# Optimization experiments

Measured on AMD Instinct MI355X. Metric: run time of the kernel, lower is better.

Reference implementation:

```python
import jax, jax.numpy as jnp
import numpy as np

B, T, P = 32, 40, 12
E, H = 2048, 1024
A_DIM, ACT_DIM = 9, 8


def _xavier(key, shape):
    fan_out, fan_in = shape
    lim = float(np.sqrt(6.0 / (fan_in + fan_out)))
    return jax.random.uniform(key, shape, jnp.float32, -lim, lim)


def setup_inputs() -> dict:
    key = jax.random.key(0)
    ks = jax.random.split(key, 8)
    return {
        "feature": jax.random.normal(ks[0], (B, T, P, E), jnp.float32),
        "W_embed": _xavier(ks[1], (H, E)),
        "b_embed": jnp.zeros((H,), jnp.float32),
        "W_ih": _xavier(ks[2], (3 * H, H)),
        "W_hh": _xavier(ks[3], (3 * H, H)),
        "b_ih": jnp.zeros((3 * H,), jnp.float32),
        "b_hh": jnp.zeros((3 * H,), jnp.float32),
        "W_act": _xavier(ks[4], (A_DIM, H)),
        "b_act": jnp.zeros((A_DIM,), jnp.float32),
        "W_activ": _xavier(ks[5], (ACT_DIM, H)),
        "b_activ": jnp.zeros((ACT_DIM,), jnp.float32),
    }


def reference(feature, W_embed, b_embed, W_ih, W_hh, b_ih, b_hh,
              W_act, b_act, W_activ, b_activ):
    # embed: Linear + Tanh -> [B, T, P, H]
    x = jnp.tanh(jnp.einsum('btpe,he->btph', feature, W_embed) + b_embed)
    # precompute input-side GRU gates for all timesteps: [B, T, P, 3H]
    gx = jnp.einsum('btph,gh->btpg', x, W_ih) + b_ih

    def step(h, gx_t):  # h: [B, P, H], gx_t: [B, P, 3H]
        gh = jnp.einsum('bph,gh->bpg', h, W_hh) + b_hh
        xr, xz, xn = jnp.split(gx_t, 3, axis=-1)
        hr, hz, hn = jnp.split(gh, 3, axis=-1)
        r = jax.nn.sigmoid(xr + hr)
        z = jax.nn.sigmoid(xz + hz)
        n = jnp.tanh(xn + r * hn)
        h_new = (1.0 - z) * n + z * h
        return h_new, h_new

    h0 = jnp.zeros((feature.shape[0], feature.shape[2], W_hh.shape[1]), feature.dtype)
    _, hs = jax.lax.scan(step, h0, jnp.moveaxis(gx, 1, 0))  # hs: [T, B, P, H]
    hiddens = jnp.moveaxis(hs, 0, 1)  # [B, T, P, H]

    # per-person action logits; torch loop order is (batch, time, person)
    action_logits = (jnp.einsum('btph,ah->btpa', hiddens, W_act) + b_act
                     ).reshape(-1, W_act.shape[0])
    # MaxPool2d((P,1)) over person axis, then Linear
    pooled = hiddens.max(axis=2)  # [B, T, H]
    activity_logits = (jnp.einsum('bth,ah->bta', pooled, W_activ) + b_activ
                       ).reshape(-1, W_activ.shape[0])
    return action_logits, activity_logits
```

## Files before the change

### kernel.cpp

```cpp
#include <hip/hip_runtime.h>
#include <cstdint>

#define B_ 32
#define T_ 40
#define P_ 12
#define E_ 2048
#define H_ 1024
#define BP 384
#define M_ 15360

typedef _Float16 f16;
typedef _Float16 f16x8 __attribute__((ext_vector_type(8)));
typedef float f32x4 __attribute__((ext_vector_type(4)));

__device__ __forceinline__ void cp16(const void* g, void* l) {
    auto gp = (const __attribute__((address_space(1))) uint32_t*)(uintptr_t)g;
    auto lp = (__attribute__((address_space(3))) uint32_t*)(uint32_t)(uintptr_t)l;
    __builtin_amdgcn_global_load_lds(gp, lp, 16, 0, 0);
}

__device__ __forceinline__ float fast_tanh(float x) {
    return 1.f - 2.f / (__expf(2.f * x) + 1.f);
}
__device__ __forceinline__ float fast_sig(float x) {
    return 1.f / (1.f + __expf(-x));
}

__global__ __launch_bounds__(256) void cvt_f32_f16(const float* __restrict__ in,
                                                   f16* __restrict__ out, int n8) {
    int i = blockIdx.x * 256 + threadIdx.x;
    if (i >= n8) return;
    const float4* in4 = (const float4*)in;
    float4 a = in4[2 * i], b = in4[2 * i + 1];
    f16x8 o = {(f16)a.x, (f16)a.y, (f16)a.z, (f16)a.w,
               (f16)b.x, (f16)b.y, (f16)b.z, (f16)b.w};
    ((f16x8*)out)[i] = o;
}

template <int EPI>
__global__ __launch_bounds__(256) void gemm128(const f16* __restrict__ A,
                                               const f16* __restrict__ Bm,
                                               const float* __restrict__ bias,
                                               f16* __restrict__ out, int K, int N) {
    __shared__ f16 As[128 * 32];
    __shared__ f16 Bs[128 * 32];
    const int tid = threadIdx.x;
    const int w = tid >> 6, l = tid & 63;
    const int wm = w >> 1, wn = w & 1;
    const long arow0 = (long)blockIdx.x * 128;
    const long brow0 = (long)blockIdx.y * 128;
    const int srow = l >> 2, scol = (l & 3) * 8;

    f32x4 acc[4][4] = {};

    for (int k0 = 0; k0 < K; k0 += 32) {
        __syncthreads();
#pragma unroll
        for (int s = 0; s < 2; ++s) {
            int slice = w + s * 4;
            cp16(A + (arow0 + slice * 16 + srow) * (long)K + k0 + scol,
                 (void*)(As + slice * 512));
            cp16(Bm + (brow0 + slice * 16 + srow) * (long)K + k0 + scol,
                 (void*)(Bs + slice * 512));
        }
        __syncthreads();
        f16x8 af[4], bf[4];
#pragma unroll
        for (int i = 0; i < 4; ++i)
            af[i] = *(const f16x8*)(As + (wm * 64 + i * 16 + (l & 15)) * 32 + (l >> 4) * 8);
#pragma unroll
        for (int j = 0; j < 4; ++j)
            bf[j] = *(const f16x8*)(Bs + (wn * 64 + j * 16 + (l & 15)) * 32 + (l >> 4) * 8);
#pragma unroll
        for (int i = 0; i < 4; ++i)
#pragma unroll
            for (int j = 0; j < 4; ++j)
                acc[i][j] = __builtin_amdgcn_mfma_f32_16x16x32_f16(af[i], bf[j], acc[i][j], 0, 0, 0);
    }

    const int colq = l & 15, rowq = (l >> 4) * 4;
#pragma unroll
    for (int i = 0; i < 4; ++i)
#pragma unroll
        for (int j = 0; j < 4; ++j)
#pragma unroll
            for (int r = 0; r < 4; ++r) {
                long m = arow0 + wm * 64 + i * 16 + rowq + r;
                int n = (int)brow0 + wn * 64 + j * 16 + colq;
                float v = acc[i][j][r] + bias[n];
                if (EPI == 0) {
                    out[m * N + n] = (f16)fast_tanh(v);
                } else {
                    int b = (int)(m / (T_ * P_));
                    int rem = (int)(m % (T_ * P_));
                    int t = rem / P_, p = rem % P_;
                    out[((long)t * BP + b * P_ + p) * N + n] = (f16)v;
                }
            }
}

__global__ __launch_bounds__(256) void gru_step(const f16* __restrict__ h16_in,
                                                f16* __restrict__ h16_out,
                                                float* __restrict__ h32,
                                                const f16* __restrict__ Whh,
                                                const float* __restrict__ b_hh,
                                                const f16* __restrict__ gx16,
                                                f16* __restrict__ hid16, int t) {
    __shared__ f16 As[32 * 32];
    __shared__ f16 Bs[3 * 64 * 32];
    const int tid = threadIdx.x;
    const int w = tid >> 6, l = tid & 63;
    const int m0 = blockIdx.x * 32, n0 = blockIdx.y * 64;
    const int srow = l >> 2, scol = (l & 3) * 8;

    f32x4 acc[3][2] = {};

    for (int k0 = 0; k0 < H_; k0 += 32) {
        __syncthreads();
        if (w < 2)
            cp16(h16_in + (m0 + w * 16 + srow) * H_ + k0 + scol, (void*)(As + w * 512));
#pragma unroll
        for (int q3 = 0; q3 < 3; ++q3) {
            int s = w + q3 * 4;
            int g = s >> 2, q = s & 3;
            cp16(Whh + (long)(g * H_ + n0 + q * 16 + srow) * H_ + k0 + scol,
                 (void*)(Bs + (g * 64 + q * 16) * 32));
        }
        __syncthreads();
        f16x8 af[2], bf[3];
#pragma unroll
        for (int i = 0; i < 2; ++i)
            af[i] = *(const f16x8*)(As + (i * 16 + (l & 15)) * 32 + (l >> 4) * 8);
#pragma unroll
        for (int g = 0; g < 3; ++g)
            bf[g] = *(const f16x8*)(Bs + (g * 64 + w * 16 + (l & 15)) * 32 + (l >> 4) * 8);
#pragma unroll
        for (int g = 0; g < 3; ++g)
#pragma unroll
            for (int i = 0; i < 2; ++i)
                acc[g][i] = __builtin_amdgcn_mfma_f32_16x16x32_f16(af[i], bf[g], acc[g][i], 0, 0, 0);
    }

    const int col = n0 + w * 16 + (l & 15);
    const long gxbase = (long)t * BP * 3072;
    const float bhr = b_hh[col], bhz = b_hh[H_ + col], bhn = b_hh[2 * H_ + col];
#pragma unroll
    for (int i = 0; i < 2; ++i)
#pragma unroll
        for (int r = 0; r < 4; ++r) {
            int m = m0 + i * 16 + (l >> 4) * 4 + r;
            float hr = acc[0][i][r] + bhr;
            float hz = acc[1][i][r] + bhz;
            float hn = acc[2][i][r] + bhn;
            long gxrow = gxbase + (long)m * 3072;
            float xr = (float)gx16[gxrow + col];
            float xz = (float)gx16[gxrow + H_ + col];
            float xn = (float)gx16[gxrow + 2 * H_ + col];
            float rr = fast_sig(xr + hr);
            float zz = fast_sig(xz + hz);
            float nn = fast_tanh(xn + rr * hn);
            float hp = h32[m * H_ + col];
            float hnew = (1.f - zz) * nn + zz * hp;
            h32[m * H_ + col] = hnew;
            h16_out[m * H_ + col] = (f16)hnew;
            int b = m / P_, p = m % P_;
            hid16[(((long)b * T_ + t) * P_ + p) * H_ + col] = (f16)hnew;
        }
}

#define GRU_GRID 256
#define GRU_THREADS 384
#define GRU_BLDS (48 * 1024 * 2)
#define GRU_ALDS (4 * 96 * 64 * 2)
#define GRU_LDS (GRU_BLDS + GRU_ALDS)
#define FLAG_STRIDE 16

__global__ __launch_bounds__(GRU_THREADS) void gru_persistent(
        const f16* __restrict__ Whh, const float* __restrict__ bhh,
        const f16* __restrict__ gx16, f16* __restrict__ hid16,
        int* __restrict__ flags) {
    extern __shared__ char lds[];
    char* const Asb = lds + GRU_BLDS;

    const int tid = threadIdx.x;
    const int w = tid >> 6, l = tid & 63;
    const int q = l >> 4;

    const int bid = blockIdx.x;
    const int x = bid & 7;
    const int rg = x >> 1;
    const int nb = (x & 1) * 32 + (bid >> 3);
    const int m0 = rg * 96;
    const int j0 = nb * 16;

    for (int c = tid; c < 6144; c += GRU_THREADS) {
        int r = c >> 7;
        int kc = (c & 127) * 8;
        int grow = (r >> 4) * H_ + j0 + (r & 15);
        f16x8 v = *(const f16x8*)(Whh + (long)grow * H_ + kc);
        *(f16x8*)(lds + r * 2048 + ((kc * 2) ^ ((r & 7) << 4))) = v;
    }

    const int arow_l = w * 16 + (l & 15);
    int a_off[2], b_off[3][2];
#pragma unroll
    for (int sub = 0; sub < 2; ++sub) {
        a_off[sub] = arow_l * 128 + (((sub * 32 + q * 8) * 2) ^ ((arow_l & 7) << 4));
#pragma unroll
        for (int g = 0; g < 3; ++g) {
            int br = g * 16 + (l & 15);
            b_off[g][sub] = br * 2048 + (((sub * 32 + q * 8) * 2) ^ ((br & 7) << 4));
        }
    }
    const int swz = ((l & 7) ^ (l >> 3)) << 3;
    const int mA1 = m0 + w * 16 + (l >> 3);
    const int mA2 = mA1 + 8;
    const long srcA1 = ((long)(mA1 / P_) * T_ * P_ + (mA1 % P_)) * H_ + swz;
    const long srcA2 = ((long)(mA2 / P_) * T_ * P_ + (mA2 % P_)) * H_ + swz;

    const int col = j0 + (l & 15);
    const float bhr = bhh[col], bhz = bhh[H_ + col], bhn = bhh[2 * H_ + col];
    const int mrow = m0 + w * 16 + q * 4;
    long dstrow[4];
#pragma unroll
    for (int r = 0; r < 4; ++r) {
        int m = mrow + r;
        dstrow[r] = ((long)(m / P_) * T_ * P_ + (m % P_)) * H_ + col;
    }

    float hval[4] = {0.f, 0.f, 0.f, 0.f};

    f16 pgr[4], pgz[4], pgn[4];
#pragma unroll
    for (int r = 0; r < 4; ++r) {
        const long row = (long)(mrow + r) * 3072 + col;
        pgr[r] = gx16[row];
        pgz[r] = gx16[row + H_];
        pgn[r] = gx16[row + 2 * H_];
    }
    __syncthreads();

    for (int t = 0; t < T_; ++t) {
        f32x4 acc0 = {}, acc1 = {}, acc2 = {};

        if (t > 0) {
            if (w == 0) {
                const int* fp = flags + (((rg << 6) + l) * FLAG_STRIDE);
                while (__hip_atomic_load(fp, __ATOMIC_RELAXED,
                                         __HIP_MEMORY_SCOPE_AGENT) < t) {
                    __builtin_amdgcn_s_sleep(2);
                }
                __builtin_amdgcn_fence(__ATOMIC_ACQUIRE, "agent");
            }
            __syncthreads();

            const f16* __restrict__ hsrc = hid16 + (long)(t - 1) * (P_ * H_);

#pragma unroll
            for (int s = 0; s < 3; ++s) {
                char* b = Asb + s * 12288 + w * 2048;
                cp16(hsrc + srcA1 + s * 64, b);
                cp16(hsrc + srcA2 + s * 64, b + 1024);
            }

#pragma unroll
            for (int kk = 0; kk < 16; ++kk) {
                asm volatile("s_waitcnt lgkmcnt(0)" ::: "memory");
                if (kk < 13) {
                    const int s = kk + 3;
                    char* b = Asb + (s & 3) * 12288 + w * 2048;
                    cp16(hsrc + srcA1 + s * 64, b);
                    cp16(hsrc + srcA2 + s * 64, b + 1024);
                    asm volatile("s_waitcnt vmcnt(6)" ::: "memory");
                } else if (kk == 13) {
                    asm volatile("s_waitcnt vmcnt(4)" ::: "memory");
                } else if (kk == 14) {
                    asm volatile("s_waitcnt vmcnt(2)" ::: "memory");
                } else {
                    asm volatile("s_waitcnt vmcnt(0)" ::: "memory");
                }
                __builtin_amdgcn_sched_barrier(0);
                const char* Ab = Asb + (kk & 3) * 12288;
#pragma unroll
                for (int sub = 0; sub < 2; ++sub) {
                    f16x8 af  = *(const f16x8*)(Ab + a_off[sub]);
                    f16x8 bf0 = *(const f16x8*)(lds + b_off[0][sub] + kk * 128);
                    f16x8 bf1 = *(const f16x8*)(lds + b_off[1][sub] + kk * 128);
                    f16x8 bf2 = *(const f16x8*)(lds + b_off[2][sub] + kk * 128);
                    acc0 = __builtin_amdgcn_mfma_f32_16x16x32_f16(af, bf0, acc0, 0, 0, 0);
                    acc1 = __builtin_amdgcn_mfma_f32_16x16x32_f16(af, bf1, acc1, 0, 0, 0);
                    acc2 = __builtin_amdgcn_mfma_f32_16x16x32_f16(af, bf2, acc2, 0, 0, 0);
                }
            }
        }

        const long toff = (long)t * (P_ * H_);
#pragma unroll
        for (int r = 0; r < 4; ++r) {
            float hr = acc0[r] + bhr;
            float hz = acc1[r] + bhz;
            float hn = acc2[r] + bhn;
            float rr = fast_sig((float)pgr[r] + hr);
            float zz = fast_sig((float)pgz[r] + hz);
            float nn = fast_tanh((float)pgn[r] + rr * hn);
            float hnew = (1.f - zz) * nn + zz * hval[r];
            hval[r] = hnew;
            hid16[toff + dstrow[r]] = (f16)hnew;
        }

        if (t + 1 < T_) {
            const long gxb = (long)(t + 1) * BP * 3072 + col;
#pragma unroll
            for (int r = 0; r < 4; ++r) {
                const long row = gxb + (long)(mrow + r) * 3072;
                pgr[r] = gx16[row];
                pgz[r] = gx16[row + H_];
                pgn[r] = gx16[row + 2 * H_];
            }
        }

        __syncthreads();
        if (tid == 0) {
            __hip_atomic_store(flags + (((rg << 6) + nb) * FLAG_STRIDE), t + 1,
                               __ATOMIC_RELEASE, __HIP_MEMORY_SCOPE_AGENT);
        }
    }
}

__global__ __launch_bounds__(256) void logits_kernel(const f16* __restrict__ hid16,
                                                     const float* __restrict__ W_act,
                                                     const float* __restrict__ b_act,
                                                     const float* __restrict__ W_activ,
                                                     const float* __restrict__ b_activ,
                                                     float* __restrict__ out) {
    __shared__ f16 hs[P_ * H_];
    __shared__ float pooled[H_];
    const int bt = blockIdx.x;
    const int tid = threadIdx.x, w = tid >> 6, l = tid & 63;

    const f16x8* src = (const f16x8*)(hid16 + (long)bt * P_ * H_);
    f16x8* dst = (f16x8*)hs;
    for (int i = tid; i < P_ * H_ / 8; i += 256) dst[i] = src[i];
    __syncthreads();

    for (int i = tid; i < H_; i += 256) {
        float mx = (float)hs[i];
#pragma unroll
        for (int p = 1; p < P_; ++p) mx = fmaxf(mx, (float)hs[p * H_ + i]);
        pooled[i] = mx;
    }
    __syncthreads();

    for (int j = w; j < 108; j += 4) {
        int p = j / 9, a = j % 9;
        float s = 0.f;
#pragma unroll
        for (int it = 0; it < 16; ++it) {
            int idx = l + it * 64;
            s += (float)hs[p * H_ + idx] * W_act[a * H_ + idx];
        }
#pragma unroll
        for (int off = 32; off > 0; off >>= 1) s += __shfl_down(s, off);
        if (l == 0) out[((long)bt * P_ + p) * 9 + a] = s + b_act[a];
    }
    for (int j = w; j < 8; j += 4) {
        float s = 0.f;
#pragma unroll
        for (int it = 0; it < 16; ++it) {
            int idx = l + it * 64;
            s += pooled[idx] * W_activ[j * H_ + idx];
        }
#pragma unroll
        for (int off = 32; off > 0; off >>= 1) s += __shfl_down(s, off);
        if (l == 0) out[(long)M_ * 9 + (long)bt * 8 + j] = s + b_activ[j];
    }
}

extern "C" void kernel_launch(void* const* d_in, const int* in_sizes, int n_in,
                              void* d_out, int out_size, void* d_ws, size_t ws_size,
                              hipStream_t stream) {
    const float* feature = (const float*)d_in[0];
    const float* W_embed = (const float*)d_in[1];
    const float* b_embed = (const float*)d_in[2];
    const float* W_ih    = (const float*)d_in[3];
    const float* W_hh    = (const float*)d_in[4];
    const float* b_ih    = (const float*)d_in[5];
    const float* b_hh    = (const float*)d_in[6];
    const float* W_act   = (const float*)d_in[7];
    const float* b_act   = (const float*)d_in[8];
    const float* W_activ = (const float*)d_in[9];
    const float* b_activ = (const float*)d_in[10];
    float* out = (float*)d_out;

    char* ws = (char*)d_ws;
    size_t off = 0;
    auto alloc = [&](size_t bytes) {
        void* p = ws + off;
        off = (off + bytes + 255) & ~(size_t)255;
        return p;
    };
    f16*   feat16 = (f16*)alloc((size_t)M_ * E_ * 2);
    f16*   wE16   = (f16*)alloc((size_t)H_ * E_ * 2);
    f16*   wIH16  = (f16*)alloc((size_t)3 * H_ * H_ * 2);
    f16*   wHH16  = (f16*)alloc((size_t)3 * H_ * H_ * 2);
    f16*   x16    = (f16*)alloc((size_t)M_ * H_ * 2);
    f16*   gx16   = (f16*)alloc((size_t)M_ * 3 * H_ * 2);
    float* h32    = (float*)alloc((size_t)BP * H_ * 4);
    f16*   h16a   = (f16*)alloc((size_t)BP * H_ * 2);
    f16*   h16b   = (f16*)alloc((size_t)BP * H_ * 2);
    f16*   hid16  = (f16*)alloc((size_t)M_ * H_ * 2);
    int*   flags  = (int*)h32;
    (void)ws_size; (void)in_sizes; (void)n_in; (void)out_size;

    cvt_f32_f16<<<(M_ * E_) / 2048, 256, 0, stream>>>(feature, feat16, (M_ * E_) / 8);
    cvt_f32_f16<<<(H_ * E_) / 2048, 256, 0, stream>>>(W_embed, wE16, (H_ * E_) / 8);
    cvt_f32_f16<<<(3 * H_ * H_) / 2048, 256, 0, stream>>>(W_ih, wIH16, (3 * H_ * H_) / 8);
    cvt_f32_f16<<<(3 * H_ * H_) / 2048, 256, 0, stream>>>(W_hh, wHH16, (3 * H_ * H_) / 8);

    gemm128<0><<<dim3(M_ / 128, H_ / 128), 256, 0, stream>>>(feat16, wE16, b_embed, x16, E_, H_);
    gemm128<1><<<dim3(M_ / 128, (3 * H_) / 128), 256, 0, stream>>>(x16, wIH16, b_ih, gx16, H_, 3 * H_);

    hipMemsetAsync(h32, 0, (size_t)BP * H_ * 4 + (size_t)BP * H_ * 2, stream);

    (void)hipFuncSetAttribute(reinterpret_cast<const void*>(gru_persistent),
                              hipFuncAttributeMaxDynamicSharedMemorySize, GRU_LDS);
    const f16* p_whh = wHH16; const float* p_bhh = b_hh; const f16* p_gx = gx16;
    f16* p_hid = hid16; int* p_flags = flags;
    void* kargs[] = {&p_whh, &p_bhh, &p_gx, &p_hid, &p_flags};
    hipError_t cerr = hipLaunchCooperativeKernel(
        reinterpret_cast<const void*>(gru_persistent),
        dim3(GRU_GRID), dim3(GRU_THREADS), kargs, GRU_LDS, stream);
    if (cerr != hipSuccess) {
        for (int t = 0; t < T_; ++t) {
            const f16* hin = (t & 1) ? h16b : h16a;
            f16* hout = (t & 1) ? h16a : h16b;
            gru_step<<<dim3(BP / 32, H_ / 64), 256, 0, stream>>>(hin, hout, h32, wHH16, b_hh,
                                                                 gx16, hid16, t);
        }
    }

    logits_kernel<<<B_ * T_, 256, 0, stream>>>(hid16, W_act, b_act, W_activ, b_activ, out);
}
```

Before: 919.4 us.

## Double-buffer GEMM LDS loads, merge convert kernels, signal GRU flags earlier

The tiled GEMM now double-buffers its A and B tiles in LDS, prefetching the next K slice while MFMAs run on the current one. This cuts the barriers per iteration from two to one and aims to hide global-load latency. The four f32-to-f16 conversion launches are merged into one kernel to save launch overhead. In the persistent GRU, hidden-state stores become write-through and the step flag is released before the next gx prefetch, so dependent blocks can proceed sooner; the cost is double the GEMM LDS use and an explicit wait on store completion.

Result: no change. 929.5 us (+1.1%).

```diff
diff --git a/kernel.cpp b/kernel.cpp
--- a/kernel.cpp
+++ b/kernel.cpp
@@ -19,6 +19,11 @@
     __builtin_amdgcn_global_load_lds(gp, lp, 16, 0, 0);
 }
 
+__device__ __forceinline__ void store_wt(f16* p, f16 v) {
+    unsigned short u = __builtin_bit_cast(unsigned short, v);
+    asm volatile("global_store_short %0, %1, off sc0 sc1" :: "v"(p), "v"(u) : "memory");
+}
+
 __device__ __forceinline__ float fast_tanh(float x) {
     return 1.f - 2.f / (__expf(2.f * x) + 1.f);
 }
@@ -26,15 +31,28 @@
     return 1.f / (1.f + __expf(-x));
 }
 
-__global__ __launch_bounds__(256) void cvt_f32_f16(const float* __restrict__ in,
-                                                   f16* __restrict__ out, int n8) {
+#define CVT_N0 ((M_ * E_) / 8)
+#define CVT_N1 (CVT_N0 + (H_ * E_) / 8)
+#define CVT_N2 (CVT_N1 + (3 * H_ * H_) / 8)
+#define CVT_N3 (CVT_N2 + (3 * H_ * H_) / 8)
+__global__ __launch_bounds__(256) void cvt_all(const float* __restrict__ f,
+                                               const float* __restrict__ we,
+                                               const float* __restrict__ wih,
+                                               const float* __restrict__ whh,
+                                               f16* __restrict__ fo, f16* __restrict__ weo,
+                                               f16* __restrict__ wiho, f16* __restrict__ whho) {
     int i = blockIdx.x * 256 + threadIdx.x;
-    if (i >= n8) return;
-    const float4* in4 = (const float4*)in;
-    float4 a = in4[2 * i], b = in4[2 * i + 1];
+    if (i >= CVT_N3) return;
+    const float* src; f16* dst; int j;
+    if (i < CVT_N0)      { src = f;   dst = fo;   j = i; }
+    else if (i < CVT_N1) { src = we;  dst = weo;  j = i - CVT_N0; }
+    else if (i < CVT_N2) { src = wih; dst = wiho; j = i - CVT_N1; }
+    else                 { src = whh; dst = whho; j = i - CVT_N2; }
+    const float4* in4 = (const float4*)src;
+    float4 a = in4[2 * j], b = in4[2 * j + 1];
     f16x8 o = {(f16)a.x, (f16)a.y, (f16)a.z, (f16)a.w,
                (f16)b.x, (f16)b.y, (f16)b.z, (f16)b.w};
-    ((f16x8*)out)[i] = o;
+    ((f16x8*)dst)[j] = o;
 }
 
 template <int EPI>
@@ -42,8 +60,8 @@
                                                const f16* __restrict__ Bm,
                                                const float* __restrict__ bias,
                                                f16* __restrict__ out, int K, int N) {
-    __shared__ f16 As[128 * 32];
-    __shared__ f16 Bs[128 * 32];
+    __shared__ f16 As[2][128 * 32];
+    __shared__ f16 Bs[2][128 * 32];
     const int tid = threadIdx.x;
     const int w = tid >> 6, l = tid & 63;
     const int wm = w >> 1, wn = w & 1;
@@ -51,31 +69,46 @@
     const long brow0 = (long)blockIdx.y * 128;
     const int srow = l >> 2, scol = (l & 3) * 8;
 
+    const f16* aptr = A + (arow0 + srow) * (long)K + scol;
+    const f16* bptr = Bm + (brow0 + srow) * (long)K + scol;
+
     f32x4 acc[4][4] = {};
 
-    for (int k0 = 0; k0 < K; k0 += 32) {
-        __syncthreads();
-#pragma unroll
-        for (int s = 0; s < 2; ++s) {
-            int slice = w + s * 4;
-            cp16(A + (arow0 + slice * 16 + srow) * (long)K + k0 + scol,
-                 (void*)(As + slice * 512));
-            cp16(Bm + (brow0 + slice * 16 + srow) * (long)K + k0 + scol,
-                 (void*)(Bs + slice * 512));
-        }
-        __syncthreads();
+#pragma unroll
+    for (int s = 0; s < 2; ++s) {
+        int slice = w + s * 4;
+        cp16(aptr + (long)slice * 16 * K, (void*)(As[0] + slice * 512));
+        cp16(bptr + (long)slice * 16 * K, (void*)(Bs[0] + slice * 512));
+    }
+    asm volatile("s_waitcnt vmcnt(0)" ::: "memory");
+    __syncthreads();
+
+    const int nt = K >> 5;
+    for (int t = 0; t < nt; ++t) {
+        const int cur = t & 1;
+        if (t + 1 < nt) {
+            const long k0 = (long)(t + 1) << 5;
+#pragma unroll
+            for (int s = 0; s < 2; ++s) {
+                int slice = w + s * 4;
+                cp16(aptr + (long)slice * 16 * K + k0, (void*)(As[cur ^ 1] + slice * 512));
+                cp16(bptr + (long)slice * 16 * K + k0, (void*)(Bs[cur ^ 1] + slice * 512));
+            }
+        }
         f16x8 af[4], bf[4];
 #pragma unroll
         for (int i = 0; i < 4; ++i)
-            af[i] = *(const f16x8*)(As + (wm * 64 + i * 16 + (l & 15)) * 32 + (l >> 4) * 8);
+            af[i] = *(const f16x8*)(As[cur] + (wm * 64 + i * 16 + (l & 15)) * 32 + (l >> 4) * 8);
 #pragma unroll
         for (int j = 0; j < 4; ++j)
-            bf[j] = *(const f16x8*)(Bs + (wn * 64 + j * 16 + (l & 15)) * 32 + (l >> 4) * 8);
+            bf[j] = *(const f16x8*)(Bs[cur] + (wn * 64 + j * 16 + (l & 15)) * 32 + (l >> 4) * 8);
 #pragma unroll
         for (int i = 0; i < 4; ++i)
 #pragma unroll
             for (int j = 0; j < 4; ++j)
                 acc[i][j] = __builtin_amdgcn_mfma_f32_16x16x32_f16(af[i], bf[j], acc[i][j], 0, 0, 0);
+        asm volatile("s_waitcnt vmcnt(0)" ::: "memory");
+        __syncthreads();
     }
 
     const int colq = l & 15, rowq = (l >> 4) * 4;
@@ -305,7 +338,13 @@
             float nn = fast_tanh((float)pgn[r] + rr * hn);
             float hnew = (1.f - zz) * nn + zz * hval[r];
             hval[r] = hnew;
-            hid16[toff + dstrow[r]] = (f16)hnew;
+            store_wt(hid16 + toff + dstrow[r], (f16)hnew);
+        }
+        asm volatile("s_waitcnt vmcnt(0)" ::: "memory");
+        __syncthreads();
+        if (tid == 0) {
+            __hip_atomic_store(flags + (((rg << 6) + nb) * FLAG_STRIDE), t + 1,
+                               __ATOMIC_RELEASE, __HIP_MEMORY_SCOPE_AGENT);
         }
 
         if (t + 1 < T_) {
@@ -317,12 +356,6 @@
                 pgz[r] = gx16[row + H_];
                 pgn[r] = gx16[row + 2 * H_];
             }
-        }
-
-        __syncthreads();
-        if (tid == 0) {
-            __hip_atomic_store(flags + (((rg << 6) + nb) * FLAG_STRIDE), t + 1,
-                               __ATOMIC_RELEASE, __HIP_MEMORY_SCOPE_AGENT);
         }
     }
 }
@@ -412,10 +445,8 @@
     int*   flags  = (int*)h32;
     (void)ws_size; (void)in_sizes; (void)n_in; (void)out_size;
 
-    cvt_f32_f16<<<(M_ * E_) / 2048, 256, 0, stream>>>(feature, feat16, (M_ * E_) / 8);
-    cvt_f32_f16<<<(H_ * E_) / 2048, 256, 0, stream>>>(W_embed, wE16, (H_ * E_) / 8);
-    cvt_f32_f16<<<(3 * H_ * H_) / 2048, 256, 0, stream>>>(W_ih, wIH16, (3 * H_ * H_) / 8);
-    cvt_f32_f16<<<(3 * H_ * H_) / 2048, 256, 0, stream>>>(W_hh, wHH16, (3 * H_ * H_) / 8);
+    cvt_all<<<CVT_N3 / 256, 256, 0, stream>>>(feature, W_embed, W_ih, W_hh,
+                                              feat16, wE16, wIH16, wHH16);
 
     gemm128<0><<<dim3(M_ / 128, H_ / 128), 256, 0, stream>>>(feat16, wE16, b_embed, x16, E_, H_);
     gemm128<1><<<dim3(M_ / 128, (3 * H_) / 128), 256, 0, stream>>>(x16, wIH16, b_ih, gx16, H_, 3 * H_);
```
